# Kernel tuning notes

Hardware: AMD Instinct MI355X
Metric: run time of the kernel (lower is better)

## Reference

```python
import jax, jax.numpy as jnp
import numpy as np
from math import sqrt

BLOCK_SIZE = 64
NUM_STEPS = 4


def _safe_normalize(x):
    n = jnp.linalg.norm(x, axis=-1, keepdims=True)
    safe_n = jnp.where(n > 0, n, 1.0)
    return jnp.where(n > 0, x / safe_n, x)


def _safe_inv_norm(x):
    n = jnp.linalg.norm(x, axis=-1, keepdims=True)
    safe_n = jnp.where(n > 0, n, 1.0)
    return jnp.where(n > 0, 1.0 / safe_n, 0.0)


def _project(x, u):
    # einsum('...i,...j,...j->...i', x, x, u)
    return x * jnp.sum(x * u, axis=-1, keepdims=True)


def _grad(lp, rp, Q, K):
    # lp: (b,h,j,l,k)  rp: (b,h,k,j,i)  Q: (b,h,l,j,v)  K: (b,h,k,i,v)
    ls = _safe_normalize(lp)
    rs = _safe_normalize(rp)
    left = ls ** 2
    right = rs ** 2
    # d_left
    r2 = jnp.sum(right ** 2, axis=-1)  # (b,h,k,j)
    KR = jnp.einsum('bhkji,bhkiv->bhkjv', right, K)
    t2l = jnp.einsum('bhkjv,bhljv->bhjlk', KR, Q)
    dl = jnp.einsum('bhkj,bhjlk->bhjlk', r2, left) - t2l
    dl = dl * 2 * ls
    dl = dl - _project(ls, dl)
    dl = dl * _safe_inv_norm(lp)
    # d_right
    l2 = jnp.sum(left ** 2, axis=-2)  # (b,h,j,k)
    LQ = jnp.einsum('bhjlk,bhljv->bhjkv', left, Q)
    t2r = jnp.einsum('bhjkv,bhkiv->bhkji', LQ, K)
    dr = jnp.einsum('bhjk,bhkji->bhkji', l2, right) - t2r
    dr = dr * 2 * rs
    dr = dr - _project(rs, dr)
    dr = dr * _safe_inv_norm(rp)
    return dl, dr


def _get_factors(query, key, attention_scale, step_size):
    B, H, S, D = query.shape
    bs = BLOCK_SIZE
    L = S // bs  # seq_len chosen divisible by block_size -> pad_amount = 0
    q = query / sqrt(D)
    q = q * jax.nn.softplus(attention_scale)[None, :, None, None]
    Q = q.reshape(B, H, L, bs, D)
    K = key.reshape(B, H, L, bs, D)
    lp = jnp.full((B, H, bs, L, L), 1.0 / sqrt(L), dtype=query.dtype)
    rp = jnp.full((B, H, L, bs, bs), 1.0 / sqrt(bs), dtype=query.dtype)
    for s in range(NUM_STEPS):
        dl, dr = _grad(lp, rp, Q, K)
        lp = lp - jax.nn.softplus(step_size[:, 0, s])[None, :, None, None, None] * dl
        rp = rp - jax.nn.softplus(step_size[:, 1, s])[None, :, None, None, None] * dr
    left = _safe_normalize(lp) ** 2
    right = _safe_normalize(rp) ** 2
    return left, right


def setup_inputs() -> dict:
    key = jax.random.key(0)
    ks = jax.random.split(key, 5)
    B, H, S, D = 4, 12, 2048, 64
    return {
        'query': jax.random.normal(ks[0], (B, H, S, D), dtype=jnp.float32),
        'key': jax.random.normal(ks[1], (B, H, S, D), dtype=jnp.float32),
        'value': jax.random.normal(ks[2], (B, H, S, D), dtype=jnp.float32),
        'attention_scale': jax.random.normal(ks[3], (H,), dtype=jnp.float32),
        'step_size': jax.random.normal(ks[4], (H, 2, NUM_STEPS), dtype=jnp.float32),
    }


def reference(query, key, value, attention_scale, step_size):
    B, H, S, D = query.shape
    bs = BLOCK_SIZE
    L = S // bs
    left, right = _get_factors(query, key, attention_scale, step_size)
    X = value.reshape(B, H, L, bs, D)
    Y = jnp.einsum('bhkji,bhkiv->bhkjv', right, X)
    Z = jnp.einsum('bhjlk,bhkjv->bhljv', left, Y)
    return Z.reshape(B, H, S, D)
```

## Files before the change

kernel.cpp:

```cpp
#include <hip/hip_runtime.h>
#include <cmath>

#define BH_ 48
#define NH_ 12
#define SS_ 2048

__device__ __forceinline__ float softplus_f(float x) {
    return fmaxf(x, 0.0f) + log1pf(expf(-fabsf(x)));
}


__global__ __launch_bounds__(64) void kA0(const float* __restrict__ key,
                                          float* __restrict__ mean) {
    int blk = blockIdx.x; int bh = blk >> 5; int k = blk & 31;
    int t = threadIdx.x;
    const float* kb = key + ((size_t)bh * SS_ + k * 64) * 64;
    float acc = 0.f;
    #pragma unroll
    for (int i = 0; i < 64; ++i) acc += kb[i * 64 + t];
    mean[((size_t)bh * 32 + k) * 64 + t] = acc * (1.0f / 64.0f);
}

template <int STEP>
__global__ __launch_bounds__(256) void kB(const float* __restrict__ query,
                                          const float* __restrict__ attn_scale,
                                          const float* __restrict__ step_size,
                                          float* __restrict__ lp,
                                          const float* __restrict__ KR,
                                          const float* __restrict__ r2,
                                          float* __restrict__ LQ,
                                          float* __restrict__ l2) {
    int blk = blockIdx.x; int bh = blk >> 6; int j = blk & 63;
    int h = bh % NH_; int t = threadIdx.x;
    __shared__ float Qs[32][68];
    __shared__ float KRs[32][68];
    __shared__ float leS[32][33];
    __shared__ float t2S[32][33];

    float qscale = softplus_f(attn_scale[h]) * 0.125f;
    float sp0 = softplus_f(step_size[h * 8 + STEP]);

    for (int idx = t; idx < 512; idx += 256) {
        int r = idx >> 4, c4 = (idx & 15) * 4;
        float4 q = *(const float4*)&query[((size_t)bh * SS_ + r * 64 + j) * 64 + c4];
        q.x *= qscale; q.y *= qscale; q.z *= qscale; q.w *= qscale;
        *(float4*)&Qs[r][c4] = q;
        float4 kr;
        if (STEP == 0) kr = *(const float4*)&KR[((size_t)bh * 32 + r) * 64 + c4];
        else           kr = *(const float4*)&KR[((size_t)(bh * 32 + r) * 64 + j) * 64 + c4];
        *(float4*)&KRs[r][c4] = kr;
    }

    int lo = t >> 3, c0 = (t & 7) * 4;
    float lpv[4], r2v[4];
    if (STEP == 0) {
        #pragma unroll
        for (int d = 0; d < 4; ++d) { lpv[d] = 0.17677669529663687f; r2v[d] = 1.0f / 64.0f; }
    } else {
        float4 v = *(const float4*)&lp[((size_t)(bh * 64 + j)) * 1024 + lo * 32 + c0];
        lpv[0] = v.x; lpv[1] = v.y; lpv[2] = v.z; lpv[3] = v.w;
        float4 w = *(const float4*)&r2[((size_t)(bh * 64 + j)) * 32 + c0];
        r2v[0] = w.x; r2v[1] = w.y; r2v[2] = w.z; r2v[3] = w.w;
    }
    float s = lpv[0]*lpv[0] + lpv[1]*lpv[1] + lpv[2]*lpv[2] + lpv[3]*lpv[3];
    s += __shfl_xor(s, 1); s += __shfl_xor(s, 2); s += __shfl_xor(s, 4);
    float n = sqrtf(s);
    float invn = (n > 0.f) ? 1.0f / n : 0.f;
    float ls[4], le[4];
    #pragma unroll
    for (int d = 0; d < 4; ++d) {
        ls[d] = lpv[d] * invn; le[d] = ls[d] * ls[d];
        leS[lo][c0 + d] = le[d];
    }
    __syncthreads();

    {
        int ml = t >> 4, mk = t & 15;
        float a00 = 0, a01 = 0, a10 = 0, a11 = 0;
        #pragma unroll 4
        for (int v4 = 0; v4 < 16; ++v4) {
            float4 q0 = *(const float4*)&Qs[ml][v4 * 4];
            float4 q1 = *(const float4*)&Qs[ml + 16][v4 * 4];
            float4 r0 = *(const float4*)&KRs[mk][v4 * 4];
            float4 r1 = *(const float4*)&KRs[mk + 16][v4 * 4];
            a00 += q0.x*r0.x + q0.y*r0.y + q0.z*r0.z + q0.w*r0.w;
            a01 += q0.x*r1.x + q0.y*r1.y + q0.z*r1.z + q0.w*r1.w;
            a10 += q1.x*r0.x + q1.y*r0.y + q1.z*r0.z + q1.w*r0.w;
            a11 += q1.x*r1.x + q1.y*r1.y + q1.z*r1.z + q1.w*r1.w;
        }
        t2S[ml][mk] = a00; t2S[ml][mk + 16] = a01;
        t2S[ml + 16][mk] = a10; t2S[ml + 16][mk + 16] = a11;
    }
    __syncthreads();

    {
        float dl[4]; float rd = 0.f;
        #pragma unroll
        for (int d = 0; d < 4; ++d) {
            float t2 = t2S[lo][c0 + d];
            dl[d] = 2.f * ls[d] * (r2v[d] * le[d] - t2);
            rd += ls[d] * dl[d];
        }
        rd += __shfl_xor(rd, 1); rd += __shfl_xor(rd, 2); rd += __shfl_xor(rd, 4);
        float4 outv;
        outv.x = lpv[0] - sp0 * ((dl[0] - ls[0] * rd) * invn);
        outv.y = lpv[1] - sp0 * ((dl[1] - ls[1] * rd) * invn);
        outv.z = lpv[2] - sp0 * ((dl[2] - ls[2] * rd) * invn);
        outv.w = lpv[3] - sp0 * ((dl[3] - ls[3] * rd) * invn);
        *(float4*)&lp[((size_t)(bh * 64 + j)) * 1024 + lo * 32 + c0] = outv;
    }

    {
        int mk = t >> 4, v0 = (t & 15) * 4;
        float4 b0 = {0, 0, 0, 0}, b1 = {0, 0, 0, 0};
        #pragma unroll 4
        for (int l = 0; l < 32; ++l) {
            float e0 = leS[l][mk], e1 = leS[l][mk + 16];
            float4 q = *(const float4*)&Qs[l][v0];
            b0.x += e0 * q.x; b0.y += e0 * q.y; b0.z += e0 * q.z; b0.w += e0 * q.w;
            b1.x += e1 * q.x; b1.y += e1 * q.y; b1.z += e1 * q.z; b1.w += e1 * q.w;
        }
        float* LQj = LQ + ((size_t)(bh * 64 + j)) * 2048;
        *(float4*)&LQj[mk * 64 + v0] = b0;
        *(float4*)&LQj[(mk + 16) * 64 + v0] = b1;
    }

    if (t < 64) {
        int k = t & 31, hh = t >> 5;
        float s2 = 0.f;
        #pragma unroll
        for (int l = hh * 16; l < hh * 16 + 16; ++l) { float x = leS[l][k]; s2 += x * x; }
        s2 += __shfl_xor(s2, 32);
        if (hh == 0) l2[(bh * 32 + k) * 64 + j] = s2;
    }
}

template <int STEP>
__global__ __launch_bounds__(256) void kCA(const float* __restrict__ key,
                                           const float* __restrict__ value,
                                           const float* __restrict__ step_size,
                                           float* __restrict__ rp,
                                           const float* __restrict__ LQ,
                                           const float* __restrict__ l2,
                                           float* __restrict__ KR,
                                           float* __restrict__ r2) {
    int blk = blockIdx.x; int bh = blk >> 5; int k = blk & 31;
    int h = bh % NH_; int t = threadIdx.x;
    __shared__ float kS[64][68];
    __shared__ float lqS[64][68];
    __shared__ float l2S[64];

    float sp1 = softplus_f(step_size[h * 8 + 4 + STEP]);
    float* rpk = rp + ((size_t)(bh * 32 + k)) * 4096;

    for (int idx = t; idx < 1024; idx += 256) {
        int r = idx >> 4, c4 = (idx & 15) * 4;
        *(float4*)&kS[r][c4]  = *(const float4*)&key[((size_t)bh * SS_ + k * 64 + r) * 64 + c4];
        *(float4*)&lqS[r][c4] = *(const float4*)&LQ[((size_t)(bh * 64 + r) * 32 + k) * 64 + c4];
    }
    if (t < 64) l2S[t] = l2[(bh * 32 + k) * 64 + t];

    int jo = t >> 2, c0 = (t & 3) * 16;
    float rv[16];
    if (STEP == 0) {
        #pragma unroll
        for (int i = 0; i < 16; ++i) rv[i] = 0.125f;
    } else {
        #pragma unroll
        for (int q4 = 0; q4 < 4; ++q4) {
            float4 v = *(const float4*)&rpk[jo * 64 + c0 + q4 * 4];
            rv[q4 * 4] = v.x; rv[q4 * 4 + 1] = v.y; rv[q4 * 4 + 2] = v.z; rv[q4 * 4 + 3] = v.w;
        }
    }
    float s2 = 0.f;
    #pragma unroll
    for (int i = 0; i < 16; ++i) s2 += rv[i] * rv[i];
    s2 += __shfl_xor(s2, 1); s2 += __shfl_xor(s2, 2);
    float n = sqrtf(s2);
    float invn = (n > 0.f) ? 1.0f / n : 0.f;
    __syncthreads();

    int mi = t & 15, mj = t >> 4;
    float acc[4][4] = {};
    #pragma unroll 2
    for (int v4 = 0; v4 < 16; ++v4) {
        float4 lq[4], kk[4];
        #pragma unroll
        for (int d = 0; d < 4; ++d) lq[d] = *(const float4*)&lqS[mj + 16 * d][v4 * 4];
        #pragma unroll
        for (int d = 0; d < 4; ++d) kk[d] = *(const float4*)&kS[mi + 16 * d][v4 * 4];
        #pragma unroll
        for (int a = 0; a < 4; ++a)
            #pragma unroll
            for (int b = 0; b < 4; ++b)
                acc[a][b] += lq[a].x * kk[b].x + lq[a].y * kk[b].y +
                             lq[a].z * kk[b].z + lq[a].w * kk[b].w;
    }
    __syncthreads();
    #pragma unroll
    for (int a = 0; a < 4; ++a)
        #pragma unroll
        for (int b = 0; b < 4; ++b) lqS[mj + 16 * a][mi + 16 * b] = acc[a][b];
    if (STEP == 3) {
        for (int idx = t; idx < 1024; idx += 256) {
            int r = idx >> 4, c4 = (idx & 15) * 4;
            *(float4*)&kS[r][c4] = *(const float4*)&value[((size_t)bh * SS_ + k * 64 + r) * 64 + c4];
        }
    }
    __syncthreads();

    float dv[16];
    #pragma unroll
    for (int q4 = 0; q4 < 4; ++q4) {
        float4 v = *(const float4*)&lqS[jo][c0 + q4 * 4];
        dv[q4 * 4] = v.x; dv[q4 * 4 + 1] = v.y; dv[q4 * 4 + 2] = v.z; dv[q4 * 4 + 3] = v.w;
    }
    float l2j = l2S[jo];
    float dot = 0.f;
    #pragma unroll
    for (int i = 0; i < 16; ++i) {
        float rs = rv[i] * invn;
        dv[i] = 2.f * rs * (l2j * rs * rs - dv[i]);
        dot += rs * dv[i];
    }
    dot += __shfl_xor(dot, 1); dot += __shfl_xor(dot, 2);
    float s2n = 0.f, s4n = 0.f;
    #pragma unroll
    for (int i = 0; i < 16; ++i) {
        float rs = rv[i] * invn;
        float d = (dv[i] - rs * dot) * invn;
        rv[i] -= sp1 * d;
        float x2 = rv[i] * rv[i];
        s2n += x2; s4n += x2 * x2;
    }
    s2n += __shfl_xor(s2n, 1); s2n += __shfl_xor(s2n, 2);
    s4n += __shfl_xor(s4n, 1); s4n += __shfl_xor(s4n, 2);
    float nn = sqrtf(s2n);
    float inn = (nn > 0.f) ? 1.0f / nn : 0.f;
    if (STEP < 3) {
        #pragma unroll
        for (int q4 = 0; q4 < 4; ++q4) {
            float4 v = make_float4(rv[q4*4], rv[q4*4+1], rv[q4*4+2], rv[q4*4+3]);
            *(float4*)&rpk[jo * 64 + c0 + q4 * 4] = v;
        }
        if ((t & 3) == 0) {
            float i2 = inn * inn;
            r2[(bh * 64 + jo) * 32 + k] = i2 * i2 * s4n;
        }
    }
    __syncthreads();

    #pragma unroll
    for (int q4 = 0; q4 < 4; ++q4) {
        float4 w;
        float a0 = rv[q4*4] * inn, a1 = rv[q4*4+1] * inn, a2 = rv[q4*4+2] * inn, a3 = rv[q4*4+3] * inn;
        w.x = a0 * a0; w.y = a1 * a1; w.z = a2 * a2; w.w = a3 * a3;
        *(float4*)&lqS[jo][c0 + q4 * 4] = w;
    }
    __syncthreads();

    {
        float4 oc[4] = {{0,0,0,0}, {0,0,0,0}, {0,0,0,0}, {0,0,0,0}};
        int v0 = mi * 4;
        #pragma unroll 2
        for (int i4 = 0; i4 < 16; ++i4) {
            float4 k0 = *(const float4*)&kS[i4 * 4 + 0][v0];
            float4 k1 = *(const float4*)&kS[i4 * 4 + 1][v0];
            float4 k2 = *(const float4*)&kS[i4 * 4 + 2][v0];
            float4 k3 = *(const float4*)&kS[i4 * 4 + 3][v0];
            #pragma unroll
            for (int a = 0; a < 4; ++a) {
                float4 rg = *(const float4*)&lqS[mj + 16 * a][i4 * 4];
                oc[a].x += rg.x * k0.x + rg.y * k1.x + rg.z * k2.x + rg.w * k3.x;
                oc[a].y += rg.x * k0.y + rg.y * k1.y + rg.z * k2.y + rg.w * k3.y;
                oc[a].z += rg.x * k0.z + rg.y * k1.z + rg.z * k2.z + rg.w * k3.z;
                oc[a].w += rg.x * k0.w + rg.y * k1.w + rg.z * k2.w + rg.w * k3.w;
            }
        }
        float* KRk = KR + ((size_t)(bh * 32 + k)) * 4096;
        #pragma unroll
        for (int a = 0; a < 4; ++a)
            *(float4*)&KRk[(mj + 16 * a) * 64 + v0] = oc[a];
    }
}

__global__ __launch_bounds__(256) void kZ(const float* __restrict__ lp,
                                          const float* Y,
                                          float* out) {
    int blk = blockIdx.x; int bh = blk >> 6; int j = blk & 63;
    int t = threadIdx.x;
    __shared__ float Ys[32][68];
    __shared__ float leS[32][33];

    for (int idx = t; idx < 512; idx += 256) {
        int r = idx >> 4, c4 = (idx & 15) * 4;
        *(float4*)&Ys[r][c4] = *(const float4*)&Y[((size_t)(bh * 32 + r) * 64 + j) * 64 + c4];
    }
    int lo = t >> 3, c0 = (t & 7) * 4;
    float4 v = *(const float4*)&lp[((size_t)(bh * 64 + j)) * 1024 + lo * 32 + c0];
    float s = v.x*v.x + v.y*v.y + v.z*v.z + v.w*v.w;
    s += __shfl_xor(s, 1); s += __shfl_xor(s, 2); s += __shfl_xor(s, 4);
    float n = sqrtf(s);
    float invn = (n > 0.f) ? 1.0f / n : 0.f;
    float a0 = v.x * invn, a1 = v.y * invn, a2 = v.z * invn, a3 = v.w * invn;
    leS[lo][c0] = a0 * a0; leS[lo][c0 + 1] = a1 * a1;
    leS[lo][c0 + 2] = a2 * a2; leS[lo][c0 + 3] = a3 * a3;
    __syncthreads();

    {
        int ml = t >> 4, v0 = (t & 15) * 4;
        float4 b0 = {0, 0, 0, 0}, b1 = {0, 0, 0, 0};
        #pragma unroll 4
        for (int kk = 0; kk < 32; ++kk) {
            float e0 = leS[ml][kk], e1 = leS[ml + 16][kk];
            float4 y = *(const float4*)&Ys[kk][v0];
            b0.x += e0 * y.x; b0.y += e0 * y.y; b0.z += e0 * y.z; b0.w += e0 * y.w;
            b1.x += e1 * y.x; b1.y += e1 * y.y; b1.z += e1 * y.z; b1.w += e1 * y.w;
        }
        *(float4*)&out[((size_t)bh * SS_ + ml * 64 + j) * 64 + v0] = b0;
        *(float4*)&out[((size_t)bh * SS_ + (ml + 16) * 64 + j) * 64 + v0] = b1;
    }
}

extern "C" void kernel_launch(void* const* d_in, const int* in_sizes, int n_in,
                              void* d_out, int out_size, void* d_ws, size_t ws_size,
                              hipStream_t stream) {
    const float* query = (const float*)d_in[0];
    const float* key   = (const float*)d_in[1];
    const float* value = (const float*)d_in[2];
    const float* attn  = (const float*)d_in[3];
    const float* ss    = (const float*)d_in[4];
    float* out = (float*)d_out;

    const size_t n_lp = (size_t)BH_ * 64 * 32 * 32;
    const size_t n_rp = (size_t)BH_ * 32 * 64 * 64;
    const size_t n_LQ = (size_t)BH_ * 64 * 32 * 64;
    const size_t n_r2 = (size_t)BH_ * 64 * 32;
    const size_t n_l2 = (size_t)BH_ * 32 * 64;
    const size_t need = (n_lp + n_rp + n_LQ + n_r2 + n_l2) * sizeof(float);
    if (ws_size < need) return;

    float* ws = (float*)d_ws;
    float* lp = ws;
    float* rp = lp + n_lp;
    float* LQ = rp + n_rp;
    float* r2 = LQ + n_LQ;
    float* l2 = r2 + n_r2;
    float* KR = out;
    float* mean = r2;

    dim3 blkD(256);
    const int gK = BH_ * 32;
    const int gJ = BH_ * 64;

    kA0<<<gK, dim3(64), 0, stream>>>(key, mean);
    kB<0><<<gJ, blkD, 0, stream>>>(query, attn, ss, lp, mean, r2, LQ, l2);
    kCA<0><<<gK, blkD, 0, stream>>>(key, value, ss, rp, LQ, l2, KR, r2);
    kB<1><<<gJ, blkD, 0, stream>>>(query, attn, ss, lp, KR, r2, LQ, l2);
    kCA<1><<<gK, blkD, 0, stream>>>(key, value, ss, rp, LQ, l2, KR, r2);
    kB<2><<<gJ, blkD, 0, stream>>>(query, attn, ss, lp, KR, r2, LQ, l2);
    kCA<2><<<gK, blkD, 0, stream>>>(key, value, ss, rp, LQ, l2, KR, r2);
    kB<3><<<gJ, blkD, 0, stream>>>(query, attn, ss, lp, KR, r2, LQ, l2);
    kCA<3><<<gK, blkD, 0, stream>>>(key, value, ss, rp, LQ, l2, KR, r2);
    kZ<<<gJ, blkD, 0, stream>>>(lp, KR, out);
}
```

Baseline: 376.9 us.

## Use split-bf16 MFMA emulation for fp32 matmuls in all kernels

Replaces the scalar FP32 FMA inner products in kB, kCA and kZ with MFMA 16x16x32 bf16 instructions. Each fp32 operand is split into three bf16 pieces (hi/mid/lo), and six cross-products are accumulated to keep roughly fp32 accuracy. Operands are staged in LDS as split bf16 arrays, transposed where needed. This adds splitting ALU work and a larger LDS footprint (a 55KB pool in kCA) in exchange for using the matrix cores. The risks are lower occupancy and small numerical differences.

```diff
diff --git a/kernel.cpp b/kernel.cpp
--- a/kernel.cpp
+++ b/kernel.cpp
@@ -5,8 +5,37 @@
 #define NH_ 12
 #define SS_ 2048
 
+typedef __attribute__((ext_vector_type(8))) short s8v;
+typedef __attribute__((ext_vector_type(4))) float f4v;
+typedef unsigned short u16;
+typedef unsigned int u32;
+
 __device__ __forceinline__ float softplus_f(float x) {
     return fmaxf(x, 0.0f) + log1pf(expf(-fabsf(x)));
+}
+
+__device__ __forceinline__ void split3(float x, u16& h, u16& m, u16& l) {
+    u32 u = __float_as_uint(x);
+    h = (u16)(u >> 16);
+    float r1 = x - __uint_as_float(u & 0xFFFF0000u);
+    u32 u1 = __float_as_uint(r1);
+    m = (u16)(u1 >> 16);
+    float r2 = r1 - __uint_as_float(u1 & 0xFFFF0000u);
+    l = (u16)(__float_as_uint(r2) >> 16);
+}
+
+__device__ __forceinline__ f4v mm6(s8v ah, s8v am, s8v al, s8v bh, s8v bm, s8v bl, f4v acc) {
+    acc = __builtin_amdgcn_mfma_f32_16x16x32_bf16(ah, bh, acc, 0, 0, 0);
+    acc = __builtin_amdgcn_mfma_f32_16x16x32_bf16(ah, bm, acc, 0, 0, 0);
+    acc = __builtin_amdgcn_mfma_f32_16x16x32_bf16(am, bh, acc, 0, 0, 0);
+    acc = __builtin_amdgcn_mfma_f32_16x16x32_bf16(ah, bl, acc, 0, 0, 0);
+    acc = __builtin_amdgcn_mfma_f32_16x16x32_bf16(al, bh, acc, 0, 0, 0);
+    acc = __builtin_amdgcn_mfma_f32_16x16x32_bf16(am, bm, acc, 0, 0, 0);
+    return acc;
+}
+
+__device__ __forceinline__ float fget(const float4& v, int q) {
+    return (q == 0) ? v.x : (q == 1) ? v.y : (q == 2) ? v.z : v.w;
 }
 
 
@@ -32,32 +61,70 @@
                                           float* __restrict__ l2) {
     int blk = blockIdx.x; int bh = blk >> 6; int j = blk & 63;
     int h = bh % NH_; int t = threadIdx.x;
-    __shared__ float Qs[32][68];
-    __shared__ float KRs[32][68];
+    __shared__ __align__(16) short Qh[32][72], Qm[32][72], Ql[32][72];
+    __shared__ __align__(16) short QTh[64][40], QTm[64][40], QTl[64][40];
+    __shared__ __align__(16) short Rh[32][72], Rm[32][72], Rl[32][72];
+    __shared__ __align__(16) short Th[32][40], Tm[32][40], Tl[32][40];
     __shared__ float leS[32][33];
-    __shared__ float t2S[32][33];
+    __shared__ float t2S[32][36];
 
     float qscale = softplus_f(attn_scale[h]) * 0.125f;
     float sp0 = softplus_f(step_size[h * 8 + STEP]);
 
-    for (int idx = t; idx < 512; idx += 256) {
-        int r = idx >> 4, c4 = (idx & 15) * 4;
-        float4 q = *(const float4*)&query[((size_t)bh * SS_ + r * 64 + j) * 64 + c4];
-        q.x *= qscale; q.y *= qscale; q.z *= qscale; q.w *= qscale;
-        *(float4*)&Qs[r][c4] = q;
-        float4 kr;
-        if (STEP == 0) kr = *(const float4*)&KR[((size_t)bh * 32 + r) * 64 + c4];
-        else           kr = *(const float4*)&KR[((size_t)(bh * 32 + r) * 64 + j) * 64 + c4];
-        *(float4*)&KRs[r][c4] = kr;
+    if (t < 128) {
+        int l0 = 4 * (t >> 4), v0 = 4 * (t & 15);
+        float4 x[4];
+        #pragma unroll
+        for (int r = 0; r < 4; ++r) {
+            x[r] = *(const float4*)&query[((size_t)bh * SS_ + (l0 + r) * 64 + j) * 64 + v0];
+            x[r].x *= qscale; x[r].y *= qscale; x[r].z *= qscale; x[r].w *= qscale;
+        }
+        u16 hh[4][4], mm[4][4], ll[4][4];
+        #pragma unroll
+        for (int r = 0; r < 4; ++r) {
+            split3(x[r].x, hh[r][0], mm[r][0], ll[r][0]);
+            split3(x[r].y, hh[r][1], mm[r][1], ll[r][1]);
+            split3(x[r].z, hh[r][2], mm[r][2], ll[r][2]);
+            split3(x[r].w, hh[r][3], mm[r][3], ll[r][3]);
+        }
+        #pragma unroll
+        for (int r = 0; r < 4; ++r) {
+            *(short4*)&Qh[l0 + r][v0] = make_short4(hh[r][0], hh[r][1], hh[r][2], hh[r][3]);
+            *(short4*)&Qm[l0 + r][v0] = make_short4(mm[r][0], mm[r][1], mm[r][2], mm[r][3]);
+            *(short4*)&Ql[l0 + r][v0] = make_short4(ll[r][0], ll[r][1], ll[r][2], ll[r][3]);
+        }
+        #pragma unroll
+        for (int q = 0; q < 4; ++q) {
+            *(short4*)&QTh[v0 + q][l0] = make_short4(hh[0][q], hh[1][q], hh[2][q], hh[3][q]);
+            *(short4*)&QTm[v0 + q][l0] = make_short4(mm[0][q], mm[1][q], mm[2][q], mm[3][q]);
+            *(short4*)&QTl[v0 + q][l0] = make_short4(ll[0][q], ll[1][q], ll[2][q], ll[3][q]);
+        }
+    } else {
+        int tt = t & 127;
+        #pragma unroll
+        for (int it = 0; it < 4; ++it) {
+            int idx = tt + 128 * it;
+            int r = idx >> 4, c4 = (idx & 15) * 4;
+            float4 x;
+            if (STEP == 0) x = *(const float4*)&KR[((size_t)bh * 32 + r) * 64 + c4];
+            else           x = *(const float4*)&KR[((size_t)(bh * 32 + r) * 64 + j) * 64 + c4];
+            u16 h0, m0_, l0_, h1, m1, l1, h2, m2, l2_, h3, m3, l3;
+            split3(x.x, h0, m0_, l0_); split3(x.y, h1, m1, l1);
+            split3(x.z, h2, m2, l2_); split3(x.w, h3, m3, l3);
+            *(short4*)&Rh[r][c4] = make_short4(h0, h1, h2, h3);
+            *(short4*)&Rm[r][c4] = make_short4(m0_, m1, m2, m3);
+            *(short4*)&Rl[r][c4] = make_short4(l0_, l1, l2_, l3);
+        }
     }
 
     int lo = t >> 3, c0 = (t & 7) * 4;
+    float* lpj = lp + ((size_t)(bh * 64 + j)) * 1024;
     float lpv[4], r2v[4];
     if (STEP == 0) {
         #pragma unroll
         for (int d = 0; d < 4; ++d) { lpv[d] = 0.17677669529663687f; r2v[d] = 1.0f / 64.0f; }
     } else {
-        float4 v = *(const float4*)&lp[((size_t)(bh * 64 + j)) * 1024 + lo * 32 + c0];
+        float4 v = *(const float4*)&lpj[lo * 32 + c0];
         lpv[0] = v.x; lpv[1] = v.y; lpv[2] = v.z; lpv[3] = v.w;
         float4 w = *(const float4*)&r2[((size_t)(bh * 64 + j)) * 32 + c0];
         r2v[0] = w.x; r2v[1] = w.y; r2v[2] = w.z; r2v[3] = w.w;
@@ -71,25 +138,57 @@
     for (int d = 0; d < 4; ++d) {
         ls[d] = lpv[d] * invn; le[d] = ls[d] * ls[d];
         leS[lo][c0 + d] = le[d];
-    }
-    __syncthreads();
+        u16 eh, em, el;
+        split3(le[d], eh, em, el);
+        Th[c0 + d][lo] = (short)eh; Tm[c0 + d][lo] = (short)em; Tl[c0 + d][lo] = (short)el;
+    }
+    __syncthreads();
+
+    int w = t >> 6, lane = t & 63;
+    int fr = lane & 15, fk = (lane >> 4) * 8;
 
     {
-        int ml = t >> 4, mk = t & 15;
-        float a00 = 0, a01 = 0, a10 = 0, a11 = 0;
-        #pragma unroll 4
-        for (int v4 = 0; v4 < 16; ++v4) {
-            float4 q0 = *(const float4*)&Qs[ml][v4 * 4];
-            float4 q1 = *(const float4*)&Qs[ml + 16][v4 * 4];
-            float4 r0 = *(const float4*)&KRs[mk][v4 * 4];
-            float4 r1 = *(const float4*)&KRs[mk + 16][v4 * 4];
-            a00 += q0.x*r0.x + q0.y*r0.y + q0.z*r0.z + q0.w*r0.w;
-            a01 += q0.x*r1.x + q0.y*r1.y + q0.z*r1.z + q0.w*r1.w;
-            a10 += q1.x*r0.x + q1.y*r0.y + q1.z*r0.z + q1.w*r0.w;
-            a11 += q1.x*r1.x + q1.y*r1.y + q1.z*r1.z + q1.w*r1.w;
-        }
-        t2S[ml][mk] = a00; t2S[ml][mk + 16] = a01;
-        t2S[ml + 16][mk] = a10; t2S[ml + 16][mk + 16] = a11;
+        int m0 = (w >> 1) * 16, n0 = (w & 1) * 16;
+        f4v acc = {0, 0, 0, 0};
+        #pragma unroll
+        for (int k0 = 0; k0 < 64; k0 += 32) {
+            s8v ah = *(const s8v*)&Qh[m0 + fr][k0 + fk];
+            s8v am = *(const s8v*)&Qm[m0 + fr][k0 + fk];
+            s8v al = *(const s8v*)&Ql[m0 + fr][k0 + fk];
+            s8v bh_ = *(const s8v*)&Rh[n0 + fr][k0 + fk];
+            s8v bm_ = *(const s8v*)&Rm[n0 + fr][k0 + fk];
+            s8v bl_ = *(const s8v*)&Rl[n0 + fr][k0 + fk];
+            acc = mm6(ah, am, al, bh_, bm_, bl_, acc);
+        }
+        #pragma unroll
+        for (int g = 0; g < 4; ++g) t2S[m0 + (lane >> 4) * 4 + g][n0 + fr] = acc[g];
+    }
+
+    {
+        int m0 = (w & 1) * 16, nb = (w >> 1) * 32;
+        s8v ah = *(const s8v*)&Th[m0 + fr][fk];
+        s8v am = *(const s8v*)&Tm[m0 + fr][fk];
+        s8v al = *(const s8v*)&Tl[m0 + fr][fk];
+        float* LQj = LQ + ((size_t)(bh * 64 + j)) * 2048;
+        #pragma unroll
+        for (int half = 0; half < 2; ++half) {
+            int n0 = nb + half * 16;
+            s8v bh_ = *(const s8v*)&QTh[n0 + fr][fk];
+            s8v bm_ = *(const s8v*)&QTm[n0 + fr][fk];
+            s8v bl_ = *(const s8v*)&QTl[n0 + fr][fk];
+            f4v acc = {0, 0, 0, 0};
+            acc = mm6(ah, am, al, bh_, bm_, bl_, acc);
+            #pragma unroll
+            for (int g = 0; g < 4; ++g)
+                LQj[(m0 + (lane >> 4) * 4 + g) * 64 + n0 + fr] = acc[g];
+        }
+    }
+
+    if (t < 32) {
+        float s2 = 0.f;
+        #pragma unroll
+        for (int l = 0; l < 32; ++l) { float x = leS[l][t]; s2 += x * x; }
+        l2[(bh * 32 + t) * 64 + j] = s2;
     }
     __syncthreads();
 
@@ -107,31 +206,7 @@
         outv.y = lpv[1] - sp0 * ((dl[1] - ls[1] * rd) * invn);
         outv.z = lpv[2] - sp0 * ((dl[2] - ls[2] * rd) * invn);
         outv.w = lpv[3] - sp0 * ((dl[3] - ls[3] * rd) * invn);
-        *(float4*)&lp[((size_t)(bh * 64 + j)) * 1024 + lo * 32 + c0] = outv;
-    }
-
-    {
-        int mk = t >> 4, v0 = (t & 15) * 4;
-        float4 b0 = {0, 0, 0, 0}, b1 = {0, 0, 0, 0};
-        #pragma unroll 4
-        for (int l = 0; l < 32; ++l) {
-            float e0 = leS[l][mk], e1 = leS[l][mk + 16];
-            float4 q = *(const float4*)&Qs[l][v0];
-            b0.x += e0 * q.x; b0.y += e0 * q.y; b0.z += e0 * q.z; b0.w += e0 * q.w;
-            b1.x += e1 * q.x; b1.y += e1 * q.y; b1.z += e1 * q.z; b1.w += e1 * q.w;
-        }
-        float* LQj = LQ + ((size_t)(bh * 64 + j)) * 2048;
-        *(float4*)&LQj[mk * 64 + v0] = b0;
-        *(float4*)&LQj[(mk + 16) * 64 + v0] = b1;
-    }
-
-    if (t < 64) {
-        int k = t & 31, hh = t >> 5;
-        float s2 = 0.f;
-        #pragma unroll
-        for (int l = hh * 16; l < hh * 16 + 16; ++l) { float x = leS[l][k]; s2 += x * x; }
-        s2 += __shfl_xor(s2, 32);
-        if (hh == 0) l2[(bh * 32 + k) * 64 + j] = s2;
+        *(float4*)&lpj[lo * 32 + c0] = outv;
     }
 }
 
@@ -146,19 +221,17 @@
                                            float* __restrict__ r2) {
     int blk = blockIdx.x; int bh = blk >> 5; int k = blk & 31;
     int h = bh % NH_; int t = threadIdx.x;
-    __shared__ float kS[64][68];
-    __shared__ float lqS[64][68];
-    __shared__ float l2S[64];
+    __shared__ __align__(16) char pool[55296];
+    short (*Ah)[72] = (short(*)[72])(pool);
+    short (*Am)[72] = (short(*)[72])(pool + 9216);
+    short (*Al)[72] = (short(*)[72])(pool + 18432);
+    short (*Bh)[72] = (short(*)[72])(pool + 27648);
+    short (*Bm)[72] = (short(*)[72])(pool + 36864);
+    short (*Bl)[72] = (short(*)[72])(pool + 46080);
+    float (*t2S)[66] = (float(*)[66])(pool);
 
     float sp1 = softplus_f(step_size[h * 8 + 4 + STEP]);
     float* rpk = rp + ((size_t)(bh * 32 + k)) * 4096;
-
-    for (int idx = t; idx < 1024; idx += 256) {
-        int r = idx >> 4, c4 = (idx & 15) * 4;
-        *(float4*)&kS[r][c4]  = *(const float4*)&key[((size_t)bh * SS_ + k * 64 + r) * 64 + c4];
-        *(float4*)&lqS[r][c4] = *(const float4*)&LQ[((size_t)(bh * 64 + r) * 32 + k) * 64 + c4];
-    }
-    if (t < 64) l2S[t] = l2[(bh * 32 + k) * 64 + t];
 
     int jo = t >> 2, c0 = (t & 3) * 16;
     float rv[16];
@@ -169,53 +242,86 @@
         #pragma unroll
         for (int q4 = 0; q4 < 4; ++q4) {
             float4 v = *(const float4*)&rpk[jo * 64 + c0 + q4 * 4];
-            rv[q4 * 4] = v.x; rv[q4 * 4 + 1] = v.y; rv[q4 * 4 + 2] = v.z; rv[q4 * 4 + 3] = v.w;
-        }
+            rv[q4*4] = v.x; rv[q4*4+1] = v.y; rv[q4*4+2] = v.z; rv[q4*4+3] = v.w;
+        }
+    }
+    float l2j = l2[(bh * 32 + k) * 64 + jo];
+
+    #pragma unroll
+    for (int it = 0; it < 4; ++it) {
+        int idx = t + 256 * it;
+        int r = idx >> 4, c4 = (idx & 15) * 4;
+        float4 a = *(const float4*)&LQ[((size_t)(bh * 64 + r) * 32 + k) * 64 + c4];
+        float4 b = *(const float4*)&key[((size_t)bh * SS_ + k * 64 + r) * 64 + c4];
+        u16 h0, m0_, l0_, h1, m1, l1, h2, m2, l2_, h3, m3, l3;
+        split3(a.x, h0, m0_, l0_); split3(a.y, h1, m1, l1);
+        split3(a.z, h2, m2, l2_); split3(a.w, h3, m3, l3);
+        *(short4*)&Ah[r][c4] = make_short4(h0, h1, h2, h3);
+        *(short4*)&Am[r][c4] = make_short4(m0_, m1, m2, m3);
+        *(short4*)&Al[r][c4] = make_short4(l0_, l1, l2_, l3);
+        split3(b.x, h0, m0_, l0_); split3(b.y, h1, m1, l1);
+        split3(b.z, h2, m2, l2_); split3(b.w, h3, m3, l3);
+        *(short4*)&Bh[r][c4] = make_short4(h0, h1, h2, h3);
+        *(short4*)&Bm[r][c4] = make_short4(m0_, m1, m2, m3);
+        *(short4*)&Bl[r][c4] = make_short4(l0_, l1, l2_, l3);
     }
     float s2 = 0.f;
     #pragma unroll
     for (int i = 0; i < 16; ++i) s2 += rv[i] * rv[i];
     s2 += __shfl_xor(s2, 1); s2 += __shfl_xor(s2, 2);
-    float n = sqrtf(s2);
-    float invn = (n > 0.f) ? 1.0f / n : 0.f;
-    __syncthreads();
-
-    int mi = t & 15, mj = t >> 4;
-    float acc[4][4] = {};
-    #pragma unroll 2
-    for (int v4 = 0; v4 < 16; ++v4) {
-        float4 lq[4], kk[4];
-        #pragma unroll
-        for (int d = 0; d < 4; ++d) lq[d] = *(const float4*)&lqS[mj + 16 * d][v4 * 4];
-        #pragma unroll
-        for (int d = 0; d < 4; ++d) kk[d] = *(const float4*)&kS[mi + 16 * d][v4 * 4];
-        #pragma unroll
-        for (int a = 0; a < 4; ++a)
-            #pragma unroll
-            for (int b = 0; b < 4; ++b)
-                acc[a][b] += lq[a].x * kk[b].x + lq[a].y * kk[b].y +
-                             lq[a].z * kk[b].z + lq[a].w * kk[b].w;
-    }
-    __syncthreads();
-    #pragma unroll
-    for (int a = 0; a < 4; ++a)
-        #pragma unroll
-        for (int b = 0; b < 4; ++b) lqS[mj + 16 * a][mi + 16 * b] = acc[a][b];
-    if (STEP == 3) {
-        for (int idx = t; idx < 1024; idx += 256) {
-            int r = idx >> 4, c4 = (idx & 15) * 4;
-            *(float4*)&kS[r][c4] = *(const float4*)&value[((size_t)bh * SS_ + k * 64 + r) * 64 + c4];
-        }
+    float nrm = sqrtf(s2);
+    float invn = (nrm > 0.f) ? 1.0f / nrm : 0.f;
+    __syncthreads();
+
+    int w = t >> 6, lane = t & 63;
+    int fr = lane & 15, fk = (lane >> 4) * 8;
+    int m0 = w * 16;
+
+    f4v acc0 = {0,0,0,0}, acc1 = {0,0,0,0}, acc2 = {0,0,0,0}, acc3 = {0,0,0,0};
+    #pragma unroll
+    for (int k0 = 0; k0 < 64; k0 += 32) {
+        s8v ah = *(const s8v*)&Ah[m0 + fr][k0 + fk];
+        s8v am = *(const s8v*)&Am[m0 + fr][k0 + fk];
+        s8v al = *(const s8v*)&Al[m0 + fr][k0 + fk];
+        {
+            s8v bh_ = *(const s8v*)&Bh[0 + fr][k0 + fk];
+            s8v bm_ = *(const s8v*)&Bm[0 + fr][k0 + fk];
+            s8v bl_ = *(const s8v*)&Bl[0 + fr][k0 + fk];
+            acc0 = mm6(ah, am, al, bh_, bm_, bl_, acc0);
+        }
+        {
+            s8v bh_ = *(const s8v*)&Bh[16 + fr][k0 + fk];
+            s8v bm_ = *(const s8v*)&Bm[16 + fr][k0 + fk];
+            s8v bl_ = *(const s8v*)&Bl[16 + fr][k0 + fk];
+            acc1 = mm6(ah, am, al, bh_, bm_, bl_, acc1);
+        }
+        {
+            s8v bh_ = *(const s8v*)&Bh[32 + fr][k0 + fk];
+            s8v bm_ = *(const s8v*)&Bm[32 + fr][k0 + fk];
+            s8v bl_ = *(const s8v*)&Bl[32 + fr][k0 + fk];
+            acc2 = mm6(ah, am, al, bh_, bm_, bl_, acc2);
+        }
+        {
+            s8v bh_ = *(const s8v*)&Bh[48 + fr][k0 + fk];
+            s8v bm_ = *(const s8v*)&Bm[48 + fr][k0 + fk];
+            s8v bl_ = *(const s8v*)&Bl[48 + fr][k0 + fk];
+            acc3 = mm6(ah, am, al, bh_, bm_, bl_, acc3);
+        }
+    }
+    __syncthreads();
+    #pragma unroll
+    for (int g = 0; g < 4; ++g) {
+        int rr = m0 + (lane >> 4) * 4 + g;
+        t2S[rr][0  + fr] = acc0[g];
+        t2S[rr][16 + fr] = acc1[g];
+        t2S[rr][32 + fr] = acc2[g];
+        t2S[rr][48 + fr] = acc3[g];
     }
     __syncthreads();
 
     float dv[16];
     #pragma unroll
-    for (int q4 = 0; q4 < 4; ++q4) {
-        float4 v = *(const float4*)&lqS[jo][c0 + q4 * 4];
-        dv[q4 * 4] = v.x; dv[q4 * 4 + 1] = v.y; dv[q4 * 4 + 2] = v.z; dv[q4 * 4 + 3] = v.w;
-    }
-    float l2j = l2S[jo];
+    for (int q = 0; q < 16; ++q) dv[q] = t2S[jo][c0 + q];
     float dot = 0.f;
     #pragma unroll
     for (int i = 0; i < 16; ++i) {
@@ -228,8 +334,8 @@
     #pragma unroll
     for (int i = 0; i < 16; ++i) {
         float rs = rv[i] * invn;
-        float d = (dv[i] - rs * dot) * invn;
-        rv[i] -= sp1 * d;
+        float dd = (dv[i] - rs * dot) * invn;
+        rv[i] -= sp1 * dd;
         float x2 = rv[i] * rv[i];
         s2n += x2; s4n += x2 * x2;
     }
@@ -239,10 +345,9 @@
     float inn = (nn > 0.f) ? 1.0f / nn : 0.f;
     if (STEP < 3) {
         #pragma unroll
-        for (int q4 = 0; q4 < 4; ++q4) {
-            float4 v = make_float4(rv[q4*4], rv[q4*4+1], rv[q4*4+2], rv[q4*4+3]);
-            *(float4*)&rpk[jo * 64 + c0 + q4 * 4] = v;
-        }
+        for (int q4 = 0; q4 < 4; ++q4)
+            *(float4*)&rpk[jo * 64 + c0 + q4 * 4] =
+                make_float4(rv[q4*4], rv[q4*4+1], rv[q4*4+2], rv[q4*4+3]);
         if ((t & 3) == 0) {
             float i2 = inn * inn;
             r2[(bh * 64 + jo) * 32 + k] = i2 * i2 * s4n;
@@ -252,35 +357,76 @@
 
     #pragma unroll
     for (int q4 = 0; q4 < 4; ++q4) {
-        float4 w;
-        float a0 = rv[q4*4] * inn, a1 = rv[q4*4+1] * inn, a2 = rv[q4*4+2] * inn, a3 = rv[q4*4+3] * inn;
-        w.x = a0 * a0; w.y = a1 * a1; w.z = a2 * a2; w.w = a3 * a3;
-        *(float4*)&lqS[jo][c0 + q4 * 4] = w;
-    }
-    __syncthreads();
-
+        u16 hh[4], mmx[4], llx[4];
+        #pragma unroll
+        for (int d = 0; d < 4; ++d) {
+            float rs = rv[q4*4 + d] * inn;
+            split3(rs * rs, hh[d], mmx[d], llx[d]);
+        }
+        *(short4*)&Ah[jo][c0 + q4 * 4] = make_short4(hh[0], hh[1], hh[2], hh[3]);
+        *(short4*)&Am[jo][c0 + q4 * 4] = make_short4(mmx[0], mmx[1], mmx[2], mmx[3]);
+        *(short4*)&Al[jo][c0 + q4 * 4] = make_short4(llx[0], llx[1], llx[2], llx[3]);
+    }
     {
-        float4 oc[4] = {{0,0,0,0}, {0,0,0,0}, {0,0,0,0}, {0,0,0,0}};
-        int v0 = mi * 4;
-        #pragma unroll 2
-        for (int i4 = 0; i4 < 16; ++i4) {
-            float4 k0 = *(const float4*)&kS[i4 * 4 + 0][v0];
-            float4 k1 = *(const float4*)&kS[i4 * 4 + 1][v0];
-            float4 k2 = *(const float4*)&kS[i4 * 4 + 2][v0];
-            float4 k3 = *(const float4*)&kS[i4 * 4 + 3][v0];
+        int i0 = (t & 15) * 4, v0 = (t >> 4) * 4;
+        const float* src = (STEP == 3) ? value : key;
+        float4 xr[4];
+        #pragma unroll
+        for (int r = 0; r < 4; ++r)
+            xr[r] = *(const float4*)&src[((size_t)bh * SS_ + k * 64 + i0 + r) * 64 + v0];
+        #pragma unroll
+        for (int q = 0; q < 4; ++q) {
+            u16 hh[4], mmx[4], llx[4];
             #pragma unroll
-            for (int a = 0; a < 4; ++a) {
-                float4 rg = *(const float4*)&lqS[mj + 16 * a][i4 * 4];
-                oc[a].x += rg.x * k0.x + rg.y * k1.x + rg.z * k2.x + rg.w * k3.x;
-                oc[a].y += rg.x * k0.y + rg.y * k1.y + rg.z * k2.y + rg.w * k3.y;
-                oc[a].z += rg.x * k0.z + rg.y * k1.z + rg.z * k2.z + rg.w * k3.z;
-                oc[a].w += rg.x * k0.w + rg.y * k1.w + rg.z * k2.w + rg.w * k3.w;
+            for (int r = 0; r < 4; ++r) split3(fget(xr[r], q), hh[r], mmx[r], llx[r]);
+            *(short4*)&Bh[v0 + q][i0] = make_short4(hh[0], hh[1], hh[2], hh[3]);
+            *(short4*)&Bm[v0 + q][i0] = make_short4(mmx[0], mmx[1], mmx[2], mmx[3]);
+            *(short4*)&Bl[v0 + q][i0] = make_short4(llx[0], llx[1], llx[2], llx[3]);
+        }
+    }
+    __syncthreads();
+
+    {
+        f4v oc0 = {0,0,0,0}, oc1 = {0,0,0,0}, oc2 = {0,0,0,0}, oc3 = {0,0,0,0};
+        #pragma unroll
+        for (int k0 = 0; k0 < 64; k0 += 32) {
+            s8v ah = *(const s8v*)&Ah[m0 + fr][k0 + fk];
+            s8v am = *(const s8v*)&Am[m0 + fr][k0 + fk];
+            s8v al = *(const s8v*)&Al[m0 + fr][k0 + fk];
+            {
+                s8v bh_ = *(const s8v*)&Bh[0 + fr][k0 + fk];
+                s8v bm_ = *(const s8v*)&Bm[0 + fr][k0 + fk];
+                s8v bl_ = *(const s8v*)&Bl[0 + fr][k0 + fk];
+                oc0 = mm6(ah, am, al, bh_, bm_, bl_, oc0);
             }
+            {
+                s8v bh_ = *(const s8v*)&Bh[16 + fr][k0 + fk];
+                s8v bm_ = *(const s8v*)&Bm[16 + fr][k0 + fk];
+                s8v bl_ = *(const s8v*)&Bl[16 + fr][k0 + fk];
+                oc1 = mm6(ah, am, al, bh_, bm_, bl_, oc1);
+            }
+            {
+                s8v bh_ = *(const s8v*)&Bh[32 + fr][k0 + fk];
+                s8v bm_ = *(const s8v*)&Bm[32 + fr][k0 + fk];
+                s8v bl_ = *(const s8v*)&Bl[32 + fr][k0 + fk];
+                oc2 = mm6(ah, am, al, bh_, bm_, bl_, oc2);
+            }
+            {
+                s8v bh_ = *(const s8v*)&Bh[48 + fr][k0 + fk];
+                s8v bm_ = *(const s8v*)&Bm[48 + fr][k0 + fk];
+                s8v bl_ = *(const s8v*)&Bl[48 + fr][k0 + fk];
+                oc3 = mm6(ah, am, al, bh_, bm_, bl_, oc3);
+            }
         }
         float* KRk = KR + ((size_t)(bh * 32 + k)) * 4096;
         #pragma unroll
-        for (int a = 0; a < 4; ++a)
-            *(float4*)&KRk[(mj + 16 * a) * 64 + v0] = oc[a];
+        for (int g = 0; g < 4; ++g) {
+            int rr = m0 + (lane >> 4) * 4 + g;
+            KRk[rr * 64 + 0  + fr] = oc0[g];
+            KRk[rr * 64 + 16 + fr] = oc1[g];
+            KRk[rr * 64 + 32 + fr] = oc2[g];
+            KRk[rr * 64 + 48 + fr] = oc3[g];
+        }
     }
 }
 
@@ -289,36 +435,60 @@
                                           float* out) {
     int blk = blockIdx.x; int bh = blk >> 6; int j = blk & 63;
     int t = threadIdx.x;
-    __shared__ float Ys[32][68];
-    __shared__ float leS[32][33];
-
-    for (int idx = t; idx < 512; idx += 256) {
-        int r = idx >> 4, c4 = (idx & 15) * 4;
-        *(float4*)&Ys[r][c4] = *(const float4*)&Y[((size_t)(bh * 32 + r) * 64 + j) * 64 + c4];
+    __shared__ __align__(16) short YTh[64][40], YTm[64][40], YTl[64][40];
+    __shared__ __align__(16) short Lh[32][40], Lm[32][40], Ll[32][40];
+
+    if (t < 128) {
+        int k0 = 4 * (t >> 4), v0 = 4 * (t & 15);
+        float4 x[4];
+        #pragma unroll
+        for (int r = 0; r < 4; ++r)
+            x[r] = *(const float4*)&Y[((size_t)(bh * 32 + k0 + r) * 64 + j) * 64 + v0];
+        #pragma unroll
+        for (int q = 0; q < 4; ++q) {
+            u16 hh[4], mm[4], ll[4];
+            #pragma unroll
+            for (int r = 0; r < 4; ++r) split3(fget(x[r], q), hh[r], mm[r], ll[r]);
+            *(short4*)&YTh[v0 + q][k0] = make_short4(hh[0], hh[1], hh[2], hh[3]);
+            *(short4*)&YTm[v0 + q][k0] = make_short4(mm[0], mm[1], mm[2], mm[3]);
+            *(short4*)&YTl[v0 + q][k0] = make_short4(ll[0], ll[1], ll[2], ll[3]);
+        }
     }
     int lo = t >> 3, c0 = (t & 7) * 4;
-    float4 v = *(const float4*)&lp[((size_t)(bh * 64 + j)) * 1024 + lo * 32 + c0];
+    const float* lpj = lp + ((size_t)(bh * 64 + j)) * 1024;
+    float4 v = *(const float4*)&lpj[lo * 32 + c0];
     float s = v.x*v.x + v.y*v.y + v.z*v.z + v.w*v.w;
     s += __shfl_xor(s, 1); s += __shfl_xor(s, 2); s += __shfl_xor(s, 4);
     float n = sqrtf(s);
     float invn = (n > 0.f) ? 1.0f / n : 0.f;
-    float a0 = v.x * invn, a1 = v.y * invn, a2 = v.z * invn, a3 = v.w * invn;
-    leS[lo][c0] = a0 * a0; leS[lo][c0 + 1] = a1 * a1;
-    leS[lo][c0 + 2] = a2 * a2; leS[lo][c0 + 3] = a3 * a3;
-    __syncthreads();
-
     {
-        int ml = t >> 4, v0 = (t & 15) * 4;
-        float4 b0 = {0, 0, 0, 0}, b1 = {0, 0, 0, 0};
-        #pragma unroll 4
-        for (int kk = 0; kk < 32; ++kk) {
-            float e0 = leS[ml][kk], e1 = leS[ml + 16][kk];
-            float4 y = *(const float4*)&Ys[kk][v0];
-            b0.x += e0 * y.x; b0.y += e0 * y.y; b0.z += e0 * y.z; b0.w += e0 * y.w;
-            b1.x += e1 * y.x; b1.y += e1 * y.y; b1.z += e1 * y.z; b1.w += e1 * y.w;
-        }
-        *(float4*)&out[((size_t)bh * SS_ + ml * 64 + j) * 64 + v0] = b0;
-        *(float4*)&out[((size_t)bh * SS_ + (ml + 16) * 64 + j) * 64 + v0] = b1;
+        float le[4] = {v.x * invn, v.y * invn, v.z * invn, v.w * invn};
+        u16 hh[4], mm[4], ll[4];
+        #pragma unroll
+        for (int d = 0; d < 4; ++d) split3(le[d] * le[d], hh[d], mm[d], ll[d]);
+        *(short4*)&Lh[lo][c0] = make_short4(hh[0], hh[1], hh[2], hh[3]);
+        *(short4*)&Lm[lo][c0] = make_short4(mm[0], mm[1], mm[2], mm[3]);
+        *(short4*)&Ll[lo][c0] = make_short4(ll[0], ll[1], ll[2], ll[3]);
+    }
+    __syncthreads();
+
+    int w = t >> 6, lane = t & 63;
+    int fr = lane & 15, fk = (lane >> 4) * 8;
+    int m0 = (w & 1) * 16, nb = (w >> 1) * 32;
+    s8v ah = *(const s8v*)&Lh[m0 + fr][fk];
+    s8v am = *(const s8v*)&Lm[m0 + fr][fk];
+    s8v al = *(const s8v*)&Ll[m0 + fr][fk];
+    #pragma unroll
+    for (int half = 0; half < 2; ++half) {
+        int n0 = nb + half * 16;
+        s8v bh_ = *(const s8v*)&YTh[n0 + fr][fk];
+        s8v bm_ = *(const s8v*)&YTm[n0 + fr][fk];
+        s8v bl_ = *(const s8v*)&YTl[n0 + fr][fk];
+        f4v acc = {0, 0, 0, 0};
+        acc = mm6(ah, am, al, bh_, bm_, bl_, acc);
+        #pragma unroll
+        for (int g = 0; g < 4; ++g)
+            out[((size_t)bh * SS_ + (m0 + (lane >> 4) * 4 + g) * 64 + j) * 64 + n0 + fr] = acc[g];
     }
 }
 
@@ -349,18 +519,17 @@
     float* KR = out;
     float* mean = r2;
 
-    dim3 blkD(256);
     const int gK = BH_ * 32;
     const int gJ = BH_ * 64;
 
     kA0<<<gK, dim3(64), 0, stream>>>(key, mean);
-    kB<0><<<gJ, blkD, 0, stream>>>(query, attn, ss, lp, mean, r2, LQ, l2);
-    kCA<0><<<gK, blkD, 0, stream>>>(key, value, ss, rp, LQ, l2, KR, r2);
-    kB<1><<<gJ, blkD, 0, stream>>>(query, attn, ss, lp, KR, r2, LQ, l2);
-    kCA<1><<<gK, blkD, 0, stream>>>(key, value, ss, rp, LQ, l2, KR, r2);
-    kB<2><<<gJ, blkD, 0, stream>>>(query, attn, ss, lp, KR, r2, LQ, l2);
-    kCA<2><<<gK, blkD, 0, stream>>>(key, value, ss, rp, LQ, l2, KR, r2);
-    kB<3><<<gJ, blkD, 0, stream>>>(query, attn, ss, lp, KR, r2, LQ, l2);
-    kCA<3><<<gK, blkD, 0, stream>>>(key, value, ss, rp, LQ, l2, KR, r2);
-    kZ<<<gJ, blkD, 0, stream>>>(lp, KR, out);
-}
+    kB<0><<<gJ, dim3(256), 0, stream>>>(query, attn, ss, lp, mean, r2, LQ, l2);
+    kCA<0><<<gK, dim3(256), 0, stream>>>(key, value, ss, rp, LQ, l2, KR, r2);
+    kB<1><<<gJ, dim3(256), 0, stream>>>(query, attn, ss, lp, KR, r2, LQ, l2);
+    kCA<1><<<gK, dim3(256), 0, stream>>>(key, value, ss, rp, LQ, l2, KR, r2);
+    kB<2><<<gJ, dim3(256), 0, stream>>>(query, attn, ss, lp, KR, r2, LQ, l2);
+    kCA<2><<<gK, dim3(256), 0, stream>>>(key, value, ss, rp, LQ, l2, KR, r2);
+    kB<3><<<gJ, dim3(256), 0, stream>>>(query, attn, ss, lp, KR, r2, LQ, l2);
+    kCA<3><<<gK, dim3(256), 0, stream>>>(key, value, ss, rp, LQ, l2, KR, r2);
+    kZ<<<gJ, dim3(256), 0, stream>>>(lp, KR, out);
+}
```

New measurement: 332.9 us. -11.7%, faster.
